# Kernel tuning notes

Measured on AMD Instinct MI355X. Metric: run time of the kernel, lower is better.

## Reference

```python
import jax, jax.numpy as jnp
import numpy as np

B, S, HD = 2, 2048, 2048   # batch, seq_len, hidden_dim
NH = 16                    # num_heads
DH = HD // NH              # head_dim = 128
L = 512                    # kv_latent_dim
WINDOW = 128               # sliding window size
SINKS = 16                 # persistent (attention-sink) tokens
KTOP = 64                  # dynamic top-k tokens selected outside window/sinks
FORGET_P = 0.1             # stochastic forgetting probability


def setup_inputs() -> dict:
    key = jax.random.key(0)
    ks = jax.random.split(key, 7)
    s = 0.02
    x = jax.random.normal(ks[0], (B, S, HD), jnp.float32)
    Wq = jax.random.normal(ks[1], (HD, HD), jnp.float32) * s
    Wc = jax.random.normal(ks[2], (HD, L), jnp.float32) * s   # kv_latent_proj
    Wk = jax.random.normal(ks[3], (L, HD), jnp.float32) * s   # k_proj (latent -> hidden)
    Wv = jax.random.normal(ks[4], (L, HD), jnp.float32) * s   # v_proj (latent -> hidden)
    Wo = jax.random.normal(ks[5], (HD, HD), jnp.float32) * s  # out_proj
    forget_mask = jax.random.bernoulli(ks[6], FORGET_P, (B, NH, S, S))
    return dict(x=x, Wq=Wq, Wc=Wc, Wk=Wk, Wv=Wv, Wo=Wo, forget_mask=forget_mask)


def reference(x, Wq, Wc, Wk, Wv, Wo, forget_mask):
    scale = DH ** -0.5
    # projections: queries from x, keys/values through low-rank latent
    q = (x @ Wq).reshape(B, S, NH, DH).transpose(0, 2, 1, 3)   # [B,H,S,D]
    c = x @ Wc                                                  # [B,S,L] latent KV
    k = (c @ Wk).reshape(B, S, NH, DH).transpose(0, 2, 1, 3)
    v = (c @ Wv).reshape(B, S, NH, DH).transpose(0, 2, 1, 3)

    scores = jnp.einsum('bhqd,bhkd->bhqk', q, k) * scale        # [B,H,S,S]

    i = jnp.arange(S)[:, None]
    j = jnp.arange(S)[None, :]
    causal = j <= i
    # static pattern: sink tokens + sliding window (always attended)
    base = causal & ((j < SINKS) | ((i - j) < WINDOW))          # [S,S]

    NEG = jnp.finfo(scores.dtype).min
    # candidates for dynamic top-k: causal positions NOT already in window/sinks
    cand = jnp.where(causal & ~base, scores, NEG)
    vals, idx = jax.lax.top_k(cand, KTOP)                       # [B,H,S,K]

    # scatter top-k indices into a boolean mask (invalid = NEG-filled entries)
    N = B * NH * S
    rows = jnp.arange(N)[:, None]
    tk = jnp.zeros((N, S), dtype=bool).at[rows, idx.reshape(N, KTOP)].set(
        (vals > NEG / 2).reshape(N, KTOP))
    tk = tk.reshape(B, NH, S, S)

    # stochastic forgetting applies only to the dynamically selected tokens;
    # sinks and the sliding window are never forgotten
    allowed = base[None, None] | (tk & ~forget_mask)

    attn = jax.nn.softmax(jnp.where(allowed, scores, NEG), axis=-1)
    o = jnp.einsum('bhqk,bhkd->bhqd', attn, v)                  # [B,H,S,D]
    o = o.transpose(0, 2, 1, 3).reshape(B, S, HD)
    return o @ Wo
```

## Files before the change

### kernel.cpp

```cpp
#include <hip/hip_runtime.h>

#define B_ 2
#define S_ 2048
#define HD_ 2048
#define NH_ 16
#define DH_ 128
#define L_ 512
#define WINDOW_ 128
#define SINKS_ 16
#define KTOP_ 64
#define KST 2052

typedef __attribute__((ext_vector_type(4))) float f32x4;
typedef __attribute__((ext_vector_type(2))) float f32x2;
typedef __attribute__((ext_vector_type(8))) __bf16 bf16x8;

__device__ inline unsigned short f2bf(float f) {
  unsigned int u = __float_as_uint(f);
  unsigned int r = (u + 0x7FFFu + ((u >> 16) & 1u)) >> 16;
  return (unsigned short)r;
}
__device__ inline float bf2f(unsigned short u) {
  unsigned int x = ((unsigned int)u) << 16;
  return __uint_as_float(x);
}
__device__ inline float bfLO(unsigned int u) { return __uint_as_float(u << 16); }
__device__ inline float bfHI(unsigned int u) { return __uint_as_float(u & 0xffff0000u); }
__device__ inline unsigned int mono(float f) {
  unsigned int u = __float_as_uint(f);
  return (u & 0x80000000u) ? ~u : (u | 0x80000000u);
}
__device__ inline float dq16(unsigned int k16) {
  unsigned int m = (k16 << 16) | 0x8000u;
  unsigned int u = (m & 0x80000000u) ? (m & 0x7fffffffu) : ~m;
  return __uint_as_float(u);
}
__device__ inline void gl16(const unsigned short* g, unsigned short* l) {
  __builtin_amdgcn_global_load_lds(
      (const __attribute__((address_space(1))) unsigned int*)g,
      (__attribute__((address_space(3))) unsigned int*)l, 16, 0, 0);
}

__global__ __launch_bounds__(256) void split_f32(const float* __restrict__ in,
                                                 unsigned short* __restrict__ hi,
                                                 unsigned short* __restrict__ lo,
                                                 int n) {
  int i = (blockIdx.x * 256 + threadIdx.x) * 4;
  int stride = gridDim.x * 256 * 4;
  for (; i < n; i += stride) {
    float4 v = *(const float4*)(in + i);
    ushort4 h, l;
    h.x = f2bf(v.x); l.x = f2bf(v.x - bf2f(h.x));
    h.y = f2bf(v.y); l.y = f2bf(v.y - bf2f(h.y));
    h.z = f2bf(v.z); l.z = f2bf(v.z - bf2f(h.z));
    h.w = f2bf(v.w); l.w = f2bf(v.w - bf2f(h.w));
    *(ushort4*)(hi + i) = h;
    *(ushort4*)(lo + i) = l;
  }
}

__global__ __launch_bounds__(256) void transpose_split(const float* __restrict__ W,
                                                       unsigned short* __restrict__ WTh,
                                                       unsigned short* __restrict__ WTl,
                                                       int K, int N) {
  __shared__ unsigned short th[32][33];
  __shared__ unsigned short tl[32][33];
  int n0 = blockIdx.x * 32, k0 = blockIdx.y * 32;
  int t = threadIdx.x;
  int cx = t & 31, ry = t >> 5;
#pragma unroll
  for (int it = 0; it < 4; ++it) {
    int kk = ry + it * 8;
    float v = W[(size_t)(k0 + kk) * N + n0 + cx];
    unsigned short h = f2bf(v);
    th[cx][kk] = h;
    tl[cx][kk] = f2bf(v - bf2f(h));
  }
  __syncthreads();
#pragma unroll
  for (int it = 0; it < 4; ++it) {
    int nn = ry + it * 8;
    WTh[(size_t)(n0 + nn) * K + k0 + cx] = th[nn][cx];
    WTl[(size_t)(n0 + nn) * K + k0 + cx] = tl[nn][cx];
  }
}

__global__ __launch_bounds__(256) void gemm_c64(const unsigned short* __restrict__ Ah,
                                                const unsigned short* __restrict__ Al,
                                                const unsigned short* __restrict__ Bth,
                                                const unsigned short* __restrict__ Btl,
                                                unsigned short* __restrict__ Chi,
                                                int M, int N, int K) {
  __shared__ unsigned short lAh[64 * 32];
  __shared__ unsigned short lAl[64 * 32];
  __shared__ unsigned short lBh[128 * 32];
  __shared__ unsigned short lBl[128 * 32];
  int t = threadIdx.x;
  int row0 = blockIdx.x * 64, col0 = blockIdx.y * 128;
  int w = t >> 6, lane = t & 63;
  int wm = w >> 1, wn = w & 1;
  int lr = lane & 15, g = lane >> 4;

  f32x4 acc[2][4] = {};

  for (int kt = 0; kt < K; kt += 32) {
    {
      int Lb = w * 1024;
      int L = Lb + lane * 16;
      int rr = L >> 6, kc = (L & 63) >> 1;
      size_t offA = (size_t)(row0 + rr) * K + kt + kc;
      gl16(Ah + offA, lAh + Lb / 2);
      gl16(Al + offA, lAl + Lb / 2);
      int Lb0 = (2 * w) * 1024;
      int L0 = Lb0 + lane * 16;
      int rr0 = L0 >> 6, kc0 = (L0 & 63) >> 1;
      size_t offB0 = (size_t)(col0 + rr0) * K + kt + kc0;
      gl16(Bth + offB0, lBh + Lb0 / 2);
      gl16(Btl + offB0, lBl + Lb0 / 2);
      int Lb1 = (2 * w + 1) * 1024;
      int L1 = Lb1 + lane * 16;
      int rr1 = L1 >> 6, kc1 = (L1 & 63) >> 1;
      size_t offB1 = (size_t)(col0 + rr1) * K + kt + kc1;
      gl16(Bth + offB1, lBh + Lb1 / 2);
      gl16(Btl + offB1, lBl + Lb1 / 2);
    }
    __syncthreads();
    bf16x8 afh[2], afl[2], bgh[4], bgl[4];
#pragma unroll
    for (int m = 0; m < 2; ++m) {
      afh[m] = *(const bf16x8*)&lAh[(wm * 32 + m * 16 + lr) * 32 + g * 8];
      afl[m] = *(const bf16x8*)&lAl[(wm * 32 + m * 16 + lr) * 32 + g * 8];
    }
#pragma unroll
    for (int n = 0; n < 4; ++n) {
      bgh[n] = *(const bf16x8*)&lBh[(wn * 64 + n * 16 + lr) * 32 + g * 8];
      bgl[n] = *(const bf16x8*)&lBl[(wn * 64 + n * 16 + lr) * 32 + g * 8];
    }
#pragma unroll
    for (int m = 0; m < 2; ++m)
#pragma unroll
      for (int n = 0; n < 4; ++n) {
        acc[m][n] = __builtin_amdgcn_mfma_f32_16x16x32_bf16(afh[m], bgh[n], acc[m][n], 0, 0, 0);
        acc[m][n] = __builtin_amdgcn_mfma_f32_16x16x32_bf16(afh[m], bgl[n], acc[m][n], 0, 0, 0);
        acc[m][n] = __builtin_amdgcn_mfma_f32_16x16x32_bf16(afl[m], bgh[n], acc[m][n], 0, 0, 0);
      }
    __syncthreads();
  }

#pragma unroll
  for (int m = 0; m < 2; ++m)
#pragma unroll
    for (int n = 0; n < 4; ++n)
#pragma unroll
      for (int r2 = 0; r2 < 4; ++r2) {
        int row = row0 + wm * 32 + m * 16 + g * 4 + r2;
        int col = col0 + wn * 64 + n * 16 + lr;
        Chi[(size_t)row * N + col] = f2bf(acc[m][n][r2]);
      }
}

__global__ __launch_bounds__(256) void gemm_1term(const unsigned short* __restrict__ Ah,
                                                  const unsigned short* __restrict__ Bth,
                                                  unsigned short* __restrict__ Chi,
                                                  int M, int N, int K, float oscale) {
  __shared__ unsigned short lA[128 * 32];
  __shared__ unsigned short lB[128 * 32];
  int t = threadIdx.x;
  int row0 = blockIdx.x * 128, col0 = blockIdx.y * 128;
  int w = t >> 6, lane = t & 63;
  int wm = w >> 1, wn = w & 1;
  int lr = lane & 15, g = lane >> 4;

  f32x4 acc[4][4] = {};

  for (int kt = 0; kt < K; kt += 32) {
#pragma unroll
    for (int cc = 0; cc < 2; ++cc) {
      int chunk = cc * 4 + w;
      int Lb = chunk * 1024;
      int L = Lb + lane * 16;
      int rr = L >> 6;
      int kc = (L & 63) >> 1;
      size_t offA = (size_t)(row0 + rr) * K + kt + kc;
      size_t offB = (size_t)(col0 + rr) * K + kt + kc;
      gl16(Ah + offA, lA + Lb / 2);
      gl16(Bth + offB, lB + Lb / 2);
    }
    __syncthreads();
    bf16x8 af[4], bg[4];
#pragma unroll
    for (int m = 0; m < 4; ++m) af[m] = *(const bf16x8*)&lA[(wm * 64 + m * 16 + lr) * 32 + g * 8];
#pragma unroll
    for (int n = 0; n < 4; ++n) bg[n] = *(const bf16x8*)&lB[(wn * 64 + n * 16 + lr) * 32 + g * 8];
#pragma unroll
    for (int m = 0; m < 4; ++m)
#pragma unroll
      for (int n = 0; n < 4; ++n)
        acc[m][n] = __builtin_amdgcn_mfma_f32_16x16x32_bf16(af[m], bg[n], acc[m][n], 0, 0, 0);
    __syncthreads();
  }

#pragma unroll
  for (int m = 0; m < 4; ++m)
#pragma unroll
    for (int n = 0; n < 4; ++n)
#pragma unroll
      for (int r2 = 0; r2 < 4; ++r2) {
        int row = row0 + wm * 64 + m * 16 + g * 4 + r2;
        int col = col0 + wn * 64 + n * 16 + lr;
        Chi[(size_t)row * N + col] = f2bf(acc[m][n][r2] * oscale);
      }
}

__global__ __launch_bounds__(256) void gemm_2term(const unsigned short* __restrict__ Ah,
                                                  const unsigned short* __restrict__ Bth,
                                                  const unsigned short* __restrict__ Btl,
                                                  float* __restrict__ Cf,
                                                  int M, int N, int K) {
  __shared__ unsigned short lA[128 * 32];
  __shared__ unsigned short lBh[128 * 32];
  __shared__ unsigned short lBl[128 * 32];
  int t = threadIdx.x;
  int row0 = blockIdx.x * 128, col0 = blockIdx.y * 128;
  int w = t >> 6, lane = t & 63;
  int wm = w >> 1, wn = w & 1;
  int lr = lane & 15, g = lane >> 4;

  f32x4 acc[4][4] = {};

  for (int kt = 0; kt < K; kt += 32) {
#pragma unroll
    for (int cc = 0; cc < 2; ++cc) {
      int chunk = cc * 4 + w;
      int Lb = chunk * 1024;
      int L = Lb + lane * 16;
      int rr = L >> 6;
      int kc = (L & 63) >> 1;
      size_t offA = (size_t)(row0 + rr) * K + kt + kc;
      size_t offB = (size_t)(col0 + rr) * K + kt + kc;
      gl16(Ah + offA, lA + Lb / 2);
      gl16(Bth + offB, lBh + Lb / 2);
      gl16(Btl + offB, lBl + Lb / 2);
    }
    __syncthreads();
    bf16x8 af[4], bgh[4], bgl[4];
#pragma unroll
    for (int m = 0; m < 4; ++m) af[m] = *(const bf16x8*)&lA[(wm * 64 + m * 16 + lr) * 32 + g * 8];
#pragma unroll
    for (int n = 0; n < 4; ++n) {
      bgh[n] = *(const bf16x8*)&lBh[(wn * 64 + n * 16 + lr) * 32 + g * 8];
      bgl[n] = *(const bf16x8*)&lBl[(wn * 64 + n * 16 + lr) * 32 + g * 8];
    }
#pragma unroll
    for (int m = 0; m < 4; ++m)
#pragma unroll
      for (int n = 0; n < 4; ++n) {
        acc[m][n] = __builtin_amdgcn_mfma_f32_16x16x32_bf16(af[m], bgh[n], acc[m][n], 0, 0, 0);
        acc[m][n] = __builtin_amdgcn_mfma_f32_16x16x32_bf16(af[m], bgl[n], acc[m][n], 0, 0, 0);
      }
    __syncthreads();
  }

#pragma unroll
  for (int m = 0; m < 4; ++m)
#pragma unroll
    for (int n = 0; n < 4; ++n)
#pragma unroll
      for (int r2 = 0; r2 < 4; ++r2) {
        int row = row0 + wm * 64 + m * 16 + g * 4 + r2;
        int col = col0 + wn * 64 + n * 16 + lr;
        Cf[(size_t)row * N + col] = acc[m][n][r2];
      }
}

__global__ __launch_bounds__(1024, 8) void attn_fused(const unsigned short* __restrict__ qh,
                                                      const unsigned short* __restrict__ kh,
                                                      const unsigned short* __restrict__ vbf,
                                                      const int* __restrict__ forget,
                                                      unsigned short* __restrict__ oh) {
  __shared__ unsigned short keys[16][KST];
  __shared__ unsigned int hist[16][128];
  __shared__ unsigned short lidx[16][224];

  int bid = blockIdx.x;
  int bh = bid >> 7;
  int tile = 127 - (bid & 127);
  int b = bh >> 4, h = bh & 15;
  int i0 = tile * 16;
  int t = threadIdx.x;
  int w = t >> 6, lane = t & 63;
  int lr = lane & 15, g = lane >> 4;

  hist[w][lane] = 0;
  hist[w][lane + 64] = 0;
  __syncthreads();

  size_t qbase = ((size_t)(b * S_ + i0 + lr)) * HD_ + h * DH_;
  bf16x8 aq[4];
#pragma unroll
  for (int ks = 0; ks < 4; ++ks) aq[ks] = *(const bf16x8*)(qh + qbase + ks * 32 + g * 8);

  for (int kblk = w; kblk <= tile; kblk += 16) {
    int j0 = kblk * 16;
    size_t kbase = ((size_t)(b * S_ + j0 + lr)) * HD_ + h * DH_;
    f32x4 acc = {0.f, 0.f, 0.f, 0.f};
#pragma unroll
    for (int ks = 0; ks < 4; ++ks) {
      bf16x8 bk = *(const bf16x8*)(kh + kbase + ks * 32 + g * 8);
      acc = __builtin_amdgcn_mfma_f32_16x16x32_bf16(aq[ks], bk, acc, 0, 0, 0);
    }
    int j = j0 + lr;
#pragma unroll
    for (int r2 = 0; r2 < 4; ++r2) {
      int rr = g * 4 + r2;
      unsigned int k16 = mono(acc[r2]) >> 16;
      keys[rr][j] = (unsigned short)k16;
      int irow = i0 + rr;
      if (j >= SINKS_ && j <= irow - WINDOW_) {
        unsigned int bkt = k16 >> 8;
        atomicAdd(&hist[rr][bkt >> 1], 1u << ((bkt & 1u) * 16));
      }
    }
  }
  __syncthreads();

  int r = w;
  int i = i0 + r;
  size_t rsg = (size_t)bh * S_ + i;

  int hi = i - WINDOW_;
  int C = hi - SINKS_ + 1;
  int mode = (C <= 0) ? 0 : (C <= KTOP_ ? 1 : 2);
  unsigned int T16 = 0; int neq = 0;

  if (mode == 2) {
    int cmax = hi >> 6;
    unsigned int need = KTOP_;
    unsigned int d0_, d1_;
    {
      unsigned int w0 = hist[r][lane * 2], w1 = hist[r][lane * 2 + 1];
      unsigned int s0 = (w0 & 0xffffu) + (w0 >> 16) + (w1 & 0xffffu) + (w1 >> 16);
      unsigned int suf = s0;
#pragma unroll
      for (int off = 1; off < 64; off <<= 1) {
        unsigned int vv = __shfl_down(suf, off);
        if (lane + off < 64) suf += vv;
      }
      unsigned int sufn = __shfl_down(suf, 1);
      if (lane == 63) sufn = 0;
      bool pl = (suf >= need) && (sufn < need);
      unsigned long long bal = __ballot(pl);
      int gg = __ffsll(bal) - 1;
      unsigned int basec = __shfl(sufn, gg);
      unsigned int cum = basec; int dstar = 4 * gg;
#pragma unroll
      for (int dd = 3; dd >= 0; --dd) {
        int d = 4 * gg + dd;
        unsigned int hd = (hist[r][d >> 1] >> ((d & 1) * 16)) & 0xffffu;
        cum += hd;
        if (cum >= need) { dstar = d; break; }
      }
      unsigned int hstar = (hist[r][dstar >> 1] >> ((dstar & 1) * 16)) & 0xffffu;
      need -= (cum - hstar);
      d0_ = (unsigned int)dstar;
    }
    hist[r][lane] = 0; hist[r][lane + 64] = 0;
    for (int c = 0; c <= cmax; ++c) {
      int j = c * 64 + lane;
      unsigned int key = keys[r][j];
      bool cand = (j >= SINKS_) && (j <= hi);
      if (cand && (key >> 8) == d0_) {
        unsigned int bkt = key & 255u;
        atomicAdd(&hist[r][bkt >> 1], 1u << ((bkt & 1u) * 16));
      }
    }
    {
      unsigned int w0 = hist[r][lane * 2], w1 = hist[r][lane * 2 + 1];
      unsigned int s0 = (w0 & 0xffffu) + (w0 >> 16) + (w1 & 0xffffu) + (w1 >> 16);
      unsigned int suf = s0;
#pragma unroll
      for (int off = 1; off < 64; off <<= 1) {
        unsigned int vv = __shfl_down(suf, off);
        if (lane + off < 64) suf += vv;
      }
      unsigned int sufn = __shfl_down(suf, 1);
      if (lane == 63) sufn = 0;
      bool pl = (suf >= need) && (sufn < need);
      unsigned long long bal = __ballot(pl);
      int gg = __ffsll(bal) - 1;
      unsigned int basec = __shfl(sufn, gg);
      unsigned int cum = basec; int dstar = 4 * gg;
#pragma unroll
      for (int dd = 3; dd >= 0; --dd) {
        int d = 4 * gg + dd;
        unsigned int hd = (hist[r][d >> 1] >> ((d & 1) * 16)) & 0xffffu;
        cum += hd;
        if (cum >= need) { dstar = d; break; }
      }
      unsigned int hstar = (hist[r][dstar >> 1] >> ((dstar & 1) * 16)) & 0xffffu;
      need -= (cum - hstar);
      d1_ = (unsigned int)dstar;
    }
    T16 = (d0_ << 8) | d1_;
    neq = (int)need;
  }

  int neq_run = neq;
  int cnt = 0;
  int nch = i >> 6;
  for (int c = 0; c <= nch; ++c) {
    int j = c * 64 + lane;
    bool valid = j <= i;
    unsigned int k16 = keys[r][j];
    bool isbase = valid && ((j < SINKS_) || ((i - j) < WINDOW_));
    bool iscand = valid && !isbase;
    bool sel = false, iseq = false;
    if (iscand) {
      if (mode == 1) sel = true;
      else if (mode == 2) {
        sel = k16 > T16;
        iseq = (k16 == T16);
      }
    }
    unsigned long long em = __ballot(iseq);
    if (iseq) {
      int rk = __popcll(em & ((1ull << lane) - 1ull));
      if (rk < neq_run) sel = true;
    }
    int taken = __popcll(em);
    neq_run -= (taken < neq_run) ? taken : neq_run;
    bool allowed = isbase || sel;
    unsigned long long am = __ballot(allowed);
    if (allowed) {
      int pos = cnt + __popcll(am & ((1ull << lane) - 1ull));
      lidx[r][pos] = (unsigned short)j;
    }
    cnt += __popcll(am);
  }

  {
    const int* frow = forget + rsg * (size_t)S_;
    int newcnt = 0;
    for (int c0 = 0; c0 < cnt; c0 += 64) {
      int p = c0 + lane;
      bool active = p < cnt;
      int j = active ? (int)lidx[r][p] : 0;
      bool isb = (j < SINKS_) || ((i - j) < WINDOW_);
      bool fbit = false;
      if (active && !isb) fbit = (frow[j] != 0);
      bool keep = active && !fbit;
      unsigned long long km = __ballot(keep);
      if (keep) {
        int npos = newcnt + __popcll(km & ((1ull << lane) - 1ull));
        lidx[r][npos] = (unsigned short)j;
      }
      newcnt += __popcll(km);
    }
    cnt = newcnt;
  }

  float sum = 0.f;
  for (int p = lane; p < cnt; p += 64) {
    int j = lidx[r][p];
    float wgt = __expf(dq16(keys[r][j]));
    sum += wgt;
    keys[r][j] = f2bf(wgt);
  }
#pragma unroll
  for (int off = 32; off >= 1; off >>= 1) sum += __shfl_xor(sum, off);
  float inv = 1.0f / sum;

  int quarter = lane >> 4;
  int q16 = lane & 15;
  int d0 = q16 * 8;
  int p0 = (cnt * quarter) >> 2;
  int p1 = (cnt * (quarter + 1)) >> 2;
  size_t vb0 = ((size_t)(b * S_)) * HD_ + h * DH_ + d0;

  f32x2 a0 = {0.f, 0.f}, a1 = {0.f, 0.f}, a2 = {0.f, 0.f}, a3 = {0.f, 0.f};
  int p = p0;
  for (; p + 2 <= p1; p += 2) {
    int ja = lidx[r][p], jb = lidx[r][p + 1];
    float wa = bf2f(keys[r][ja]), wb = bf2f(keys[r][jb]);
    f32x2 wa2 = {wa, wa}, wb2 = {wb, wb};
    uint4 va = *(const uint4*)(vbf + vb0 + (size_t)ja * HD_);
    uint4 vb = *(const uint4*)(vbf + vb0 + (size_t)jb * HD_);
    f32x2 ea0 = {bfLO(va.x), bfHI(va.x)}, eb0 = {bfLO(vb.x), bfHI(vb.x)};
    f32x2 ea1 = {bfLO(va.y), bfHI(va.y)}, eb1 = {bfLO(vb.y), bfHI(vb.y)};
    f32x2 ea2 = {bfLO(va.z), bfHI(va.z)}, eb2 = {bfLO(vb.z), bfHI(vb.z)};
    f32x2 ea3 = {bfLO(va.w), bfHI(va.w)}, eb3 = {bfLO(vb.w), bfHI(vb.w)};
    a0 += wa2 * ea0 + wb2 * eb0;
    a1 += wa2 * ea1 + wb2 * eb1;
    a2 += wa2 * ea2 + wb2 * eb2;
    a3 += wa2 * ea3 + wb2 * eb3;
  }
  for (; p < p1; ++p) {
    int j = lidx[r][p];
    float wj = bf2f(keys[r][j]);
    f32x2 w2 = {wj, wj};
    uint4 vj = *(const uint4*)(vbf + vb0 + (size_t)j * HD_);
    f32x2 e0 = {bfLO(vj.x), bfHI(vj.x)};
    f32x2 e1 = {bfLO(vj.y), bfHI(vj.y)};
    f32x2 e2 = {bfLO(vj.z), bfHI(vj.z)};
    f32x2 e3 = {bfLO(vj.w), bfHI(vj.w)};
    a0 += w2 * e0; a1 += w2 * e1; a2 += w2 * e2; a3 += w2 * e3;
  }
#pragma unroll
  for (int off = 16; off <= 32; off <<= 1) {
    a0.x += __shfl_xor(a0.x, off); a0.y += __shfl_xor(a0.y, off);
    a1.x += __shfl_xor(a1.x, off); a1.y += __shfl_xor(a1.y, off);
    a2.x += __shfl_xor(a2.x, off); a2.y += __shfl_xor(a2.y, off);
    a3.x += __shfl_xor(a3.x, off); a3.y += __shfl_xor(a3.y, off);
  }
  if (quarter == 0) {
    ushort4 h0, h1;
    h0.x = f2bf(a0.x * inv); h0.y = f2bf(a0.y * inv);
    h0.z = f2bf(a1.x * inv); h0.w = f2bf(a1.y * inv);
    h1.x = f2bf(a2.x * inv); h1.y = f2bf(a2.y * inv);
    h1.z = f2bf(a3.x * inv); h1.w = f2bf(a3.y * inv);
    size_t oidx = ((size_t)(b * S_ + i)) * HD_ + h * DH_ + d0;
    *(ushort4*)(oh + oidx) = h0;
    *(ushort4*)(oh + oidx + 4) = h1;
  }
}

extern "C" void kernel_launch(void* const* d_in, const int* in_sizes, int n_in,
                              void* d_out, int out_size, void* d_ws, size_t ws_size,
                              hipStream_t stream) {
  (void)in_sizes; (void)n_in; (void)out_size; (void)ws_size;
  const float* x  = (const float*)d_in[0];
  const float* Wq = (const float*)d_in[1];
  const float* Wc = (const float*)d_in[2];
  const float* Wk = (const float*)d_in[3];
  const float* Wv = (const float*)d_in[4];
  const float* Wo = (const float*)d_in[5];
  const int* forget = (const int*)d_in[6];

  char* ws = (char*)d_ws;
  size_t off = 0;
  auto alloc = [&](size_t bytes) { char* p = ws + off; off += (bytes + 255) & ~(size_t)255; return p; };

  unsigned short* x_hi = (unsigned short*)alloc((size_t)4096 * 2048 * 2);
  unsigned short* x_lo = (unsigned short*)alloc((size_t)4096 * 2048 * 2);
  unsigned short* WqTh = (unsigned short*)alloc((size_t)2048 * 2048 * 2);
  unsigned short* WqTl = (unsigned short*)alloc((size_t)2048 * 2048 * 2);
  unsigned short* WcTh = (unsigned short*)alloc((size_t)512 * 2048 * 2);
  unsigned short* WcTl = (unsigned short*)alloc((size_t)512 * 2048 * 2);
  unsigned short* WkTh = (unsigned short*)alloc((size_t)2048 * 512 * 2);
  unsigned short* WkTl = (unsigned short*)alloc((size_t)2048 * 512 * 2);
  unsigned short* WvTh = (unsigned short*)alloc((size_t)2048 * 512 * 2);
  unsigned short* WvTl = (unsigned short*)alloc((size_t)2048 * 512 * 2);
  unsigned short* WoTh = (unsigned short*)alloc((size_t)2048 * 2048 * 2);
  unsigned short* WoTl = (unsigned short*)alloc((size_t)2048 * 2048 * 2);
  unsigned short* q_hi = (unsigned short*)alloc((size_t)4096 * 2048 * 2);
  unsigned short* c_hi = (unsigned short*)alloc((size_t)4096 * 512 * 2);
  unsigned short* k_hi = (unsigned short*)alloc((size_t)4096 * 2048 * 2);
  unsigned short* v_bf = (unsigned short*)alloc((size_t)4096 * 2048 * 2);

  unsigned short* o_hi = x_hi;

  const float scale = 0.08838834764831845f;

  split_f32<<<2048, 256, 0, stream>>>(x, x_hi, x_lo, 4096 * 2048);
  transpose_split<<<dim3(64, 64), 256, 0, stream>>>(Wq, WqTh, WqTl, 2048, 2048);
  transpose_split<<<dim3(16, 64), 256, 0, stream>>>(Wc, WcTh, WcTl, 2048, 512);
  transpose_split<<<dim3(64, 16), 256, 0, stream>>>(Wk, WkTh, WkTl, 512, 2048);
  transpose_split<<<dim3(64, 16), 256, 0, stream>>>(Wv, WvTh, WvTl, 512, 2048);
  transpose_split<<<dim3(64, 64), 256, 0, stream>>>(Wo, WoTh, WoTl, 2048, 2048);

  gemm_c64<<<dim3(64, 4), 256, 0, stream>>>(x_hi, x_lo, WcTh, WcTl, c_hi, 4096, 512, 2048);
  gemm_1term<<<dim3(32, 16), 256, 0, stream>>>(x_hi, WqTh, q_hi, 4096, 2048, 2048, scale);
  gemm_1term<<<dim3(32, 16), 256, 0, stream>>>(c_hi, WkTh, k_hi, 4096, 2048, 512, 1.0f);
  gemm_1term<<<dim3(32, 16), 256, 0, stream>>>(c_hi, WvTh, v_bf, 4096, 2048, 512, 1.0f);

  attn_fused<<<4096, 1024, 0, stream>>>(q_hi, k_hi, v_bf, forget, o_hi);

  gemm_2term<<<dim3(32, 16), 256, 0, stream>>>(o_hi, WoTh, WoTl, (float*)d_out, 4096, 2048, 2048);
}
```

Baseline: 651.7 us.

## Drop split-bf16 precision terms and fuse softmax weights into packed index list

Replaces the hi/lo bf16 split of x, Wq, Wk, Wv, Wo with single bf16 casts. This removes extra MFMA terms in the Wc and output GEMMs, the lo-buffer writes, and the extra transpose work, at the cost of lower numerical accuracy. The attention kernel now computes exp weights during selection and packs index and bf16 weight into one scratch array. Forgotten entries are subtracted from the sum afterwards instead of being handled in a separate exp pass, and the histogram and index buffers share one shared-memory array.

New measurement: 614.7 us. -5.7%, faster.

```diff
diff --git a/kernel.cpp b/kernel.cpp
--- a/kernel.cpp
+++ b/kernel.cpp
@@ -41,21 +41,36 @@
       (__attribute__((address_space(3))) unsigned int*)l, 16, 0, 0);
 }
 
-__global__ __launch_bounds__(256) void split_f32(const float* __restrict__ in,
-                                                 unsigned short* __restrict__ hi,
-                                                 unsigned short* __restrict__ lo,
-                                                 int n) {
+__global__ __launch_bounds__(256) void cast_f32(const float* __restrict__ in,
+                                                unsigned short* __restrict__ hi,
+                                                int n) {
   int i = (blockIdx.x * 256 + threadIdx.x) * 4;
   int stride = gridDim.x * 256 * 4;
   for (; i < n; i += stride) {
     float4 v = *(const float4*)(in + i);
-    ushort4 h, l;
-    h.x = f2bf(v.x); l.x = f2bf(v.x - bf2f(h.x));
-    h.y = f2bf(v.y); l.y = f2bf(v.y - bf2f(h.y));
-    h.z = f2bf(v.z); l.z = f2bf(v.z - bf2f(h.z));
-    h.w = f2bf(v.w); l.w = f2bf(v.w - bf2f(h.w));
+    ushort4 h;
+    h.x = f2bf(v.x); h.y = f2bf(v.y); h.z = f2bf(v.z); h.w = f2bf(v.w);
     *(ushort4*)(hi + i) = h;
-    *(ushort4*)(lo + i) = l;
+  }
+}
+
+__global__ __launch_bounds__(256) void transpose_cast(const float* __restrict__ W,
+                                                      unsigned short* __restrict__ WT,
+                                                      int K, int N) {
+  __shared__ unsigned short th[32][33];
+  int n0 = blockIdx.x * 32, k0 = blockIdx.y * 32;
+  int t = threadIdx.x;
+  int cx = t & 31, ry = t >> 5;
+#pragma unroll
+  for (int it = 0; it < 4; ++it) {
+    int kk = ry + it * 8;
+    th[cx][kk] = f2bf(W[(size_t)(k0 + kk) * N + n0 + cx]);
+  }
+  __syncthreads();
+#pragma unroll
+  for (int it = 0; it < 4; ++it) {
+    int nn = ry + it * 8;
+    WT[(size_t)(n0 + nn) * K + k0 + cx] = th[nn][cx];
   }
 }
 
@@ -86,13 +101,11 @@
 }
 
 __global__ __launch_bounds__(256) void gemm_c64(const unsigned short* __restrict__ Ah,
-                                                const unsigned short* __restrict__ Al,
                                                 const unsigned short* __restrict__ Bth,
                                                 const unsigned short* __restrict__ Btl,
                                                 unsigned short* __restrict__ Chi,
                                                 int M, int N, int K) {
   __shared__ unsigned short lAh[64 * 32];
-  __shared__ unsigned short lAl[64 * 32];
   __shared__ unsigned short lBh[128 * 32];
   __shared__ unsigned short lBl[128 * 32];
   int t = threadIdx.x;
@@ -110,7 +123,6 @@
       int rr = L >> 6, kc = (L & 63) >> 1;
       size_t offA = (size_t)(row0 + rr) * K + kt + kc;
       gl16(Ah + offA, lAh + Lb / 2);
-      gl16(Al + offA, lAl + Lb / 2);
       int Lb0 = (2 * w) * 1024;
       int L0 = Lb0 + lane * 16;
       int rr0 = L0 >> 6, kc0 = (L0 & 63) >> 1;
@@ -125,12 +137,10 @@
       gl16(Btl + offB1, lBl + Lb1 / 2);
     }
     __syncthreads();
-    bf16x8 afh[2], afl[2], bgh[4], bgl[4];
-#pragma unroll
-    for (int m = 0; m < 2; ++m) {
-      afh[m] = *(const bf16x8*)&lAh[(wm * 32 + m * 16 + lr) * 32 + g * 8];
-      afl[m] = *(const bf16x8*)&lAl[(wm * 32 + m * 16 + lr) * 32 + g * 8];
-    }
+    bf16x8 af[2], bgh[4], bgl[4];
+#pragma unroll
+    for (int m = 0; m < 2; ++m)
+      af[m] = *(const bf16x8*)&lAh[(wm * 32 + m * 16 + lr) * 32 + g * 8];
 #pragma unroll
     for (int n = 0; n < 4; ++n) {
       bgh[n] = *(const bf16x8*)&lBh[(wn * 64 + n * 16 + lr) * 32 + g * 8];
@@ -140,9 +150,8 @@
     for (int m = 0; m < 2; ++m)
 #pragma unroll
       for (int n = 0; n < 4; ++n) {
-        acc[m][n] = __builtin_amdgcn_mfma_f32_16x16x32_bf16(afh[m], bgh[n], acc[m][n], 0, 0, 0);
-        acc[m][n] = __builtin_amdgcn_mfma_f32_16x16x32_bf16(afh[m], bgl[n], acc[m][n], 0, 0, 0);
-        acc[m][n] = __builtin_amdgcn_mfma_f32_16x16x32_bf16(afl[m], bgh[n], acc[m][n], 0, 0, 0);
+        acc[m][n] = __builtin_amdgcn_mfma_f32_16x16x32_bf16(af[m], bgh[n], acc[m][n], 0, 0, 0);
+        acc[m][n] = __builtin_amdgcn_mfma_f32_16x16x32_bf16(af[m], bgl[n], acc[m][n], 0, 0, 0);
       }
     __syncthreads();
   }
@@ -212,14 +221,12 @@
       }
 }
 
-__global__ __launch_bounds__(256) void gemm_2term(const unsigned short* __restrict__ Ah,
-                                                  const unsigned short* __restrict__ Bth,
-                                                  const unsigned short* __restrict__ Btl,
-                                                  float* __restrict__ Cf,
-                                                  int M, int N, int K) {
+__global__ __launch_bounds__(256) void gemm_1f(const unsigned short* __restrict__ Ah,
+                                               const unsigned short* __restrict__ Bth,
+                                               float* __restrict__ Cf,
+                                               int M, int N, int K) {
   __shared__ unsigned short lA[128 * 32];
-  __shared__ unsigned short lBh[128 * 32];
-  __shared__ unsigned short lBl[128 * 32];
+  __shared__ unsigned short lB[128 * 32];
   int t = threadIdx.x;
   int row0 = blockIdx.x * 128, col0 = blockIdx.y * 128;
   int w = t >> 6, lane = t & 63;
@@ -239,25 +246,19 @@
       size_t offA = (size_t)(row0 + rr) * K + kt + kc;
       size_t offB = (size_t)(col0 + rr) * K + kt + kc;
       gl16(Ah + offA, lA + Lb / 2);
-      gl16(Bth + offB, lBh + Lb / 2);
-      gl16(Btl + offB, lBl + Lb / 2);
+      gl16(Bth + offB, lB + Lb / 2);
     }
     __syncthreads();
-    bf16x8 af[4], bgh[4], bgl[4];
+    bf16x8 af[4], bg[4];
 #pragma unroll
     for (int m = 0; m < 4; ++m) af[m] = *(const bf16x8*)&lA[(wm * 64 + m * 16 + lr) * 32 + g * 8];
 #pragma unroll
-    for (int n = 0; n < 4; ++n) {
-      bgh[n] = *(const bf16x8*)&lBh[(wn * 64 + n * 16 + lr) * 32 + g * 8];
-      bgl[n] = *(const bf16x8*)&lBl[(wn * 64 + n * 16 + lr) * 32 + g * 8];
-    }
+    for (int n = 0; n < 4; ++n) bg[n] = *(const bf16x8*)&lB[(wn * 64 + n * 16 + lr) * 32 + g * 8];
 #pragma unroll
     for (int m = 0; m < 4; ++m)
 #pragma unroll
-      for (int n = 0; n < 4; ++n) {
-        acc[m][n] = __builtin_amdgcn_mfma_f32_16x16x32_bf16(af[m], bgh[n], acc[m][n], 0, 0, 0);
-        acc[m][n] = __builtin_amdgcn_mfma_f32_16x16x32_bf16(af[m], bgl[n], acc[m][n], 0, 0, 0);
-      }
+      for (int n = 0; n < 4; ++n)
+        acc[m][n] = __builtin_amdgcn_mfma_f32_16x16x32_bf16(af[m], bg[n], acc[m][n], 0, 0, 0);
     __syncthreads();
   }
 
@@ -279,8 +280,7 @@
                                                       const int* __restrict__ forget,
                                                       unsigned short* __restrict__ oh) {
   __shared__ unsigned short keys[16][KST];
-  __shared__ unsigned int hist[16][128];
-  __shared__ unsigned short lidx[16][224];
+  __shared__ unsigned int scratch[16][224];
 
   int bid = blockIdx.x;
   int bh = bid >> 7;
@@ -291,8 +291,8 @@
   int w = t >> 6, lane = t & 63;
   int lr = lane & 15, g = lane >> 4;
 
-  hist[w][lane] = 0;
-  hist[w][lane + 64] = 0;
+  scratch[w][lane] = 0;
+  scratch[w][lane + 64] = 0;
   __syncthreads();
 
   size_t qbase = ((size_t)(b * S_ + i0 + lr)) * HD_ + h * DH_;
@@ -318,7 +318,7 @@
       int irow = i0 + rr;
       if (j >= SINKS_ && j <= irow - WINDOW_) {
         unsigned int bkt = k16 >> 8;
-        atomicAdd(&hist[rr][bkt >> 1], 1u << ((bkt & 1u) * 16));
+        atomicAdd(&scratch[rr][bkt >> 1], 1u << ((bkt & 1u) * 16));
       }
     }
   }
@@ -338,7 +338,7 @@
     unsigned int need = KTOP_;
     unsigned int d0_, d1_;
     {
-      unsigned int w0 = hist[r][lane * 2], w1 = hist[r][lane * 2 + 1];
+      unsigned int w0 = scratch[r][lane * 2], w1 = scratch[r][lane * 2 + 1];
       unsigned int s0 = (w0 & 0xffffu) + (w0 >> 16) + (w1 & 0xffffu) + (w1 >> 16);
       unsigned int suf = s0;
 #pragma unroll
@@ -356,26 +356,26 @@
 #pragma unroll
       for (int dd = 3; dd >= 0; --dd) {
         int d = 4 * gg + dd;
-        unsigned int hd = (hist[r][d >> 1] >> ((d & 1) * 16)) & 0xffffu;
+        unsigned int hd = (scratch[r][d >> 1] >> ((d & 1) * 16)) & 0xffffu;
         cum += hd;
         if (cum >= need) { dstar = d; break; }
       }
-      unsigned int hstar = (hist[r][dstar >> 1] >> ((dstar & 1) * 16)) & 0xffffu;
+      unsigned int hstar = (scratch[r][dstar >> 1] >> ((dstar & 1) * 16)) & 0xffffu;
       need -= (cum - hstar);
       d0_ = (unsigned int)dstar;
     }
-    hist[r][lane] = 0; hist[r][lane + 64] = 0;
+    scratch[r][lane] = 0; scratch[r][lane + 64] = 0;
     for (int c = 0; c <= cmax; ++c) {
       int j = c * 64 + lane;
       unsigned int key = keys[r][j];
       bool cand = (j >= SINKS_) && (j <= hi);
       if (cand && (key >> 8) == d0_) {
         unsigned int bkt = key & 255u;
-        atomicAdd(&hist[r][bkt >> 1], 1u << ((bkt & 1u) * 16));
+        atomicAdd(&scratch[r][bkt >> 1], 1u << ((bkt & 1u) * 16));
       }
     }
     {
-      unsigned int w0 = hist[r][lane * 2], w1 = hist[r][lane * 2 + 1];
+      unsigned int w0 = scratch[r][lane * 2], w1 = scratch[r][lane * 2 + 1];
       unsigned int s0 = (w0 & 0xffffu) + (w0 >> 16) + (w1 & 0xffffu) + (w1 >> 16);
       unsigned int suf = s0;
 #pragma unroll
@@ -393,11 +393,11 @@
 #pragma unroll
       for (int dd = 3; dd >= 0; --dd) {
         int d = 4 * gg + dd;
-        unsigned int hd = (hist[r][d >> 1] >> ((d & 1) * 16)) & 0xffffu;
+        unsigned int hd = (scratch[r][d >> 1] >> ((d & 1) * 16)) & 0xffffu;
         cum += hd;
         if (cum >= need) { dstar = d; break; }
       }
-      unsigned int hstar = (hist[r][dstar >> 1] >> ((dstar & 1) * 16)) & 0xffffu;
+      unsigned int hstar = (scratch[r][dstar >> 1] >> ((dstar & 1) * 16)) & 0xffffu;
       need -= (cum - hstar);
       d1_ = (unsigned int)dstar;
     }
@@ -407,6 +407,7 @@
 
   int neq_run = neq;
   int cnt = 0;
+  float sum = 0.f;
   int nch = i >> 6;
   for (int c = 0; c <= nch; ++c) {
     int j = c * 64 + lane;
@@ -430,45 +431,44 @@
     int taken = __popcll(em);
     neq_run -= (taken < neq_run) ? taken : neq_run;
     bool allowed = isbase || sel;
+    float wgt = 0.f;
+    if (allowed) { wgt = __expf(dq16(k16)); sum += wgt; }
     unsigned long long am = __ballot(allowed);
     if (allowed) {
       int pos = cnt + __popcll(am & ((1ull << lane) - 1ull));
-      lidx[r][pos] = (unsigned short)j;
+      scratch[r][pos] = ((unsigned int)j << 16) | (unsigned int)f2bf(wgt);
     }
     cnt += __popcll(am);
   }
 
+  float dropped = 0.f;
   {
     const int* frow = forget + rsg * (size_t)S_;
     int newcnt = 0;
     for (int c0 = 0; c0 < cnt; c0 += 64) {
       int p = c0 + lane;
       bool active = p < cnt;
-      int j = active ? (int)lidx[r][p] : 0;
+      unsigned int pk = active ? scratch[r][p] : 0u;
+      int j = (int)(pk >> 16);
       bool isb = (j < SINKS_) || ((i - j) < WINDOW_);
       bool fbit = false;
       if (active && !isb) fbit = (frow[j] != 0);
+      if (fbit) dropped += bf2f((unsigned short)(pk & 0xffffu));
       bool keep = active && !fbit;
       unsigned long long km = __ballot(keep);
       if (keep) {
         int npos = newcnt + __popcll(km & ((1ull << lane) - 1ull));
-        lidx[r][npos] = (unsigned short)j;
+        scratch[r][npos] = pk;
       }
       newcnt += __popcll(km);
     }
     cnt = newcnt;
   }
 
-  float sum = 0.f;
-  for (int p = lane; p < cnt; p += 64) {
-    int j = lidx[r][p];
-    float wgt = __expf(dq16(keys[r][j]));
-    sum += wgt;
-    keys[r][j] = f2bf(wgt);
-  }
-#pragma unroll
-  for (int off = 32; off >= 1; off >>= 1) sum += __shfl_xor(sum, off);
-  float inv = 1.0f / sum;
+  float s2 = sum - dropped;
+#pragma unroll
+  for (int off = 32; off >= 1; off >>= 1) s2 += __shfl_xor(s2, off);
+  float inv = 1.0f / s2;
 
   int quarter = lane >> 4;
   int q16 = lane & 15;
@@ -480,8 +480,10 @@
   f32x2 a0 = {0.f, 0.f}, a1 = {0.f, 0.f}, a2 = {0.f, 0.f}, a3 = {0.f, 0.f};
   int p = p0;
   for (; p + 2 <= p1; p += 2) {
-    int ja = lidx[r][p], jb = lidx[r][p + 1];
-    float wa = bf2f(keys[r][ja]), wb = bf2f(keys[r][jb]);
+    unsigned int pka = scratch[r][p], pkb = scratch[r][p + 1];
+    int ja = (int)(pka >> 16), jb = (int)(pkb >> 16);
+    float wa = bf2f((unsigned short)(pka & 0xffffu));
+    float wb = bf2f((unsigned short)(pkb & 0xffffu));
     f32x2 wa2 = {wa, wa}, wb2 = {wb, wb};
     uint4 va = *(const uint4*)(vbf + vb0 + (size_t)ja * HD_);
     uint4 vb = *(const uint4*)(vbf + vb0 + (size_t)jb * HD_);
@@ -495,8 +497,9 @@
     a3 += wa2 * ea3 + wb2 * eb3;
   }
   for (; p < p1; ++p) {
-    int j = lidx[r][p];
-    float wj = bf2f(keys[r][j]);
+    unsigned int pk = scratch[r][p];
+    int j = (int)(pk >> 16);
+    float wj = bf2f((unsigned short)(pk & 0xffffu));
     f32x2 w2 = {wj, wj};
     uint4 vj = *(const uint4*)(vbf + vb0 + (size_t)j * HD_);
     f32x2 e0 = {bfLO(vj.x), bfHI(vj.x)};
@@ -540,40 +543,35 @@
   size_t off = 0;
   auto alloc = [&](size_t bytes) { char* p = ws + off; off += (bytes + 255) & ~(size_t)255; return p; };
 
-  unsigned short* x_hi = (unsigned short*)alloc((size_t)4096 * 2048 * 2);
-  unsigned short* x_lo = (unsigned short*)alloc((size_t)4096 * 2048 * 2);
-  unsigned short* WqTh = (unsigned short*)alloc((size_t)2048 * 2048 * 2);
-  unsigned short* WqTl = (unsigned short*)alloc((size_t)2048 * 2048 * 2);
+  unsigned short* x_bf = (unsigned short*)alloc((size_t)4096 * 2048 * 2);
+  unsigned short* WqT  = (unsigned short*)alloc((size_t)2048 * 2048 * 2);
   unsigned short* WcTh = (unsigned short*)alloc((size_t)512 * 2048 * 2);
   unsigned short* WcTl = (unsigned short*)alloc((size_t)512 * 2048 * 2);
-  unsigned short* WkTh = (unsigned short*)alloc((size_t)2048 * 512 * 2);
-  unsigned short* WkTl = (unsigned short*)alloc((size_t)2048 * 512 * 2);
-  unsigned short* WvTh = (unsigned short*)alloc((size_t)2048 * 512 * 2);
-  unsigned short* WvTl = (unsigned short*)alloc((size_t)2048 * 512 * 2);
-  unsigned short* WoTh = (unsigned short*)alloc((size_t)2048 * 2048 * 2);
-  unsigned short* WoTl = (unsigned short*)alloc((size_t)2048 * 2048 * 2);
+  unsigned short* WkT  = (unsigned short*)alloc((size_t)2048 * 512 * 2);
+  unsigned short* WvT  = (unsigned short*)alloc((size_t)2048 * 512 * 2);
+  unsigned short* WoT  = (unsigned short*)alloc((size_t)2048 * 2048 * 2);
   unsigned short* q_hi = (unsigned short*)alloc((size_t)4096 * 2048 * 2);
   unsigned short* c_hi = (unsigned short*)alloc((size_t)4096 * 512 * 2);
   unsigned short* k_hi = (unsigned short*)alloc((size_t)4096 * 2048 * 2);
   unsigned short* v_bf = (unsigned short*)alloc((size_t)4096 * 2048 * 2);
 
-  unsigned short* o_hi = x_hi;
+  unsigned short* o_hi = x_bf;
 
   const float scale = 0.08838834764831845f;
 
-  split_f32<<<2048, 256, 0, stream>>>(x, x_hi, x_lo, 4096 * 2048);
-  transpose_split<<<dim3(64, 64), 256, 0, stream>>>(Wq, WqTh, WqTl, 2048, 2048);
+  cast_f32<<<2048, 256, 0, stream>>>(x, x_bf, 4096 * 2048);
+  transpose_cast<<<dim3(64, 64), 256, 0, stream>>>(Wq, WqT, 2048, 2048);
   transpose_split<<<dim3(16, 64), 256, 0, stream>>>(Wc, WcTh, WcTl, 2048, 512);
-  transpose_split<<<dim3(64, 16), 256, 0, stream>>>(Wk, WkTh, WkTl, 512, 2048);
-  transpose_split<<<dim3(64, 16), 256, 0, stream>>>(Wv, WvTh, WvTl, 512, 2048);
-  transpose_split<<<dim3(64, 64), 256, 0, stream>>>(Wo, WoTh, WoTl, 2048, 2048);
-
-  gemm_c64<<<dim3(64, 4), 256, 0, stream>>>(x_hi, x_lo, WcTh, WcTl, c_hi, 4096, 512, 2048);
-  gemm_1term<<<dim3(32, 16), 256, 0, stream>>>(x_hi, WqTh, q_hi, 4096, 2048, 2048, scale);
-  gemm_1term<<<dim3(32, 16), 256, 0, stream>>>(c_hi, WkTh, k_hi, 4096, 2048, 512, 1.0f);
-  gemm_1term<<<dim3(32, 16), 256, 0, stream>>>(c_hi, WvTh, v_bf, 4096, 2048, 512, 1.0f);
+  transpose_cast<<<dim3(64, 16), 256, 0, stream>>>(Wk, WkT, 512, 2048);
+  transpose_cast<<<dim3(64, 16), 256, 0, stream>>>(Wv, WvT, 512, 2048);
+  transpose_cast<<<dim3(64, 64), 256, 0, stream>>>(Wo, WoT, 2048, 2048);
+
+  gemm_c64<<<dim3(64, 4), 256, 0, stream>>>(x_bf, WcTh, WcTl, c_hi, 4096, 512, 2048);
+  gemm_1term<<<dim3(32, 16), 256, 0, stream>>>(x_bf, WqT, q_hi, 4096, 2048, 2048, scale);
+  gemm_1term<<<dim3(32, 16), 256, 0, stream>>>(c_hi, WkT, k_hi, 4096, 2048, 512, 1.0f);
+  gemm_1term<<<dim3(32, 16), 256, 0, stream>>>(c_hi, WvT, v_bf, 4096, 2048, 512, 1.0f);
 
   attn_fused<<<4096, 1024, 0, stream>>>(q_hi, k_hi, v_bf, forget, o_hi);
 
-  gemm_2term<<<dim3(32, 16), 256, 0, stream>>>(o_hi, WoTh, WoTl, (float*)d_out, 4096, 2048, 2048);
-}
+  gemm_1f<<<dim3(32, 16), 256, 0, stream>>>(o_hi, WoT, (float*)d_out, 4096, 2048, 2048);
+}
```
